# Performance work log

Measured on AMD Instinct MI355X. Metric: run time of the kernel, lower is better.

## Reference

```python
import jax, jax.numpy as jnp
import numpy as np

B, IN, H = 4096, 1024, 1024


def setup_inputs() -> dict:
    key = jax.random.key(0)
    ks = jax.random.split(key, 6)
    s_h = 1.0 / np.sqrt(H)
    s_x = 1.0 / np.sqrt(IN)
    return {
        "x": jax.random.normal(ks[0], (B, IN), jnp.float32),
        "h": jax.random.normal(ks[1], (B, H), jnp.float32),
        "c": jax.random.normal(ks[2], (B, H), jnp.float32),
        # hidden_lin: Linear(H, 4H) with bias
        "Wh": jax.random.uniform(ks[3], (4 * H, H), jnp.float32, -s_h, s_h),
        "bh": jax.random.uniform(ks[4], (4 * H,), jnp.float32, -s_h, s_h),
        # input_lin: Linear(IN, 4H), bias=False
        "Wx": jax.random.uniform(ks[5], (4 * H, IN), jnp.float32, -s_x, s_x),
    }


def reference(x, h, c, Wh, bh, Wx):
    # ifgo = h @ Wh^T + bh + x @ Wx^T   -> [B, 4H]
    ifgo = jnp.dot(h, Wh.T) + bh + jnp.dot(x, Wx.T)
    i, f, g, o = jnp.split(ifgo, 4, axis=1)
    i = jax.nn.sigmoid(i)
    f = jax.nn.sigmoid(f)
    g = jnp.tanh(g)
    o = jax.nn.sigmoid(o)
    c_next = f * c + i * g
    h_next = o * jnp.tanh(c_next)
    return (h_next, c_next)
```

## Files before the change

kernel.cpp:

```cpp
#include <hip/hip_runtime.h>
#include <cstdint>
#include <cstddef>


#define NB   4096
#define KH   1024
#define KK   2048
#define ARR_ELEMS 4194304
#define NKT  32

typedef __bf16 bf16x8 __attribute__((ext_vector_type(8)));
typedef float  f32x4  __attribute__((ext_vector_type(4)));

__device__ inline unsigned short f2bf(float f) {
    union { float f; unsigned int u; } v; v.f = f;
    unsigned int u = v.u;
    u += 0x7FFFu + ((u >> 16) & 1u);
    return (unsigned short)(u >> 16);
}

__device__ inline float fsig(float v)  { return __builtin_amdgcn_rcpf(1.f + __expf(-v)); }
__device__ inline float ftanh(float v) { return 1.f - 2.f * __builtin_amdgcn_rcpf(1.f + __expf(2.f * v)); }

__global__ void convert_kernel(const float* __restrict__ h, const float* __restrict__ x,
                               const float* __restrict__ Wh, const float* __restrict__ Wx,
                               unsigned short* __restrict__ A, unsigned short* __restrict__ W) {
    int idx = blockIdx.x * 256 + threadIdx.x;
    int arr = idx >> 19;
    int off = (idx & 0x7FFFF) << 3;
    const float* src = (arr == 0) ? h : (arr == 1) ? x : (arr == 2) ? Wh : Wx;
    float4 v0 = *(const float4*)(src + off);
    float4 v1 = *(const float4*)(src + off + 4);
    uint4 packed;
    packed.x = (unsigned int)f2bf(v0.x) | ((unsigned int)f2bf(v0.y) << 16);
    packed.y = (unsigned int)f2bf(v0.z) | ((unsigned int)f2bf(v0.w) << 16);
    packed.z = (unsigned int)f2bf(v1.x) | ((unsigned int)f2bf(v1.y) << 16);
    packed.w = (unsigned int)f2bf(v1.z) | ((unsigned int)f2bf(v1.w) << 16);

    int row = off >> 10;
    int col = off & 1023;
    unsigned short* dst;
    size_t dstOff;
    if (arr < 2) {
        dst = A;
        dstOff = (size_t)row * KK + (arr == 1 ? 1024 : 0) + col;
    } else {
        int g = row >> 10, j = row & 1023;
        int p = ((j >> 4) << 6) | (g << 4) | (j & 15);
        dst = W;
        dstOff = (size_t)p * KK + (arr == 3 ? 1024 : 0) + col;
    }
    *(uint4*)(dst + dstOff) = packed;
}

__global__ __launch_bounds__(512, 2) void gemm_kernel(const unsigned short* __restrict__ A,
                            const unsigned short* __restrict__ W,
                            const float* __restrict__ bh,
                            const float* __restrict__ c,
                            float* __restrict__ out) {
    __shared__ __align__(16) unsigned short As[2 * 16384];
    __shared__ __align__(16) unsigned short Bs[2 * 16384];

    const int tid  = threadIdx.x;
    const int wave = tid >> 6;
    const int lane = tid & 63;

    const int bid   = (int)blockIdx.x;
    const int swz   = (bid & 7) * 32 + (bid >> 3);
    const int tileM = swz >> 4;
    const int tileN = swz & 15;

    const int wr  = wave >> 2;
    const int wc  = wave & 3;
    const int fr  = lane & 15;
    const int fk2 = (lane >> 4) << 4;

    const unsigned short* pa[4];
    const unsigned short* pb[4];
    #pragma unroll
    for (int i = 0; i < 4; ++i) {
        const int P   = (i * 512 + tid) * 16;
        const int L   = P ^ (((P >> 7) & 7) << 4);
        const int row = L >> 7;
        const int kk  = (L & 127) >> 1;
        pa[i] = A + (size_t)(tileM * 256 + row) * KK + kk;
        pb[i] = W + (size_t)(tileN * 256 + row) * KK + kk;
    }

    const int swzm = (fr & 7) << 4;
    int offA[8], offB[4];
    #pragma unroll
    for (int i = 0; i < 8; ++i)
        offA[i] = (wr * 128 + i * 16 + fr) * 128 + (fk2 ^ swzm);
    #pragma unroll
    for (int j = 0; j < 4; ++j)
        offB[j] = (wc * 64 + j * 16 + fr) * 128 + (fk2 ^ swzm);

    f32x4 acc[8][4] = {};
    bf16x8 a03[4][2], a47[4][2], b01[2][2], b23[2][2];

#define STAGE(KT, BUF) do { \
    const size_t _ko = (size_t)(KT) * 64; \
    _Pragma("unroll") \
    for (int _i = 0; _i < 4; ++_i) { \
        __builtin_amdgcn_global_load_lds( \
            (const __attribute__((address_space(1))) void*)(pa[_i] + _ko), \
            (__attribute__((address_space(3))) void*)(As + (BUF) * 16384 + _i * 4096 + wave * 512), 16, 0, 0); \
        __builtin_amdgcn_global_load_lds( \
            (const __attribute__((address_space(1))) void*)(pb[_i] + _ko), \
            (__attribute__((address_space(3))) void*)(Bs + (BUF) * 16384 + _i * 4096 + wave * 512), 16, 0, 0); \
    } \
} while (0)

#define READ_A(dst, base, AsB) do { \
    _Pragma("unroll") \
    for (int _i = 0; _i < 4; ++_i) { \
        dst[_i][0] = *(const bf16x8*)((AsB) + offA[(base) + _i]); \
        dst[_i][1] = *(const bf16x8*)((AsB) + (offA[(base) + _i] ^ 64)); \
    } \
} while (0)

#define READ_B(dst, base, BsB) do { \
    _Pragma("unroll") \
    for (int _j = 0; _j < 2; ++_j) { \
        dst[_j][0] = *(const bf16x8*)((BsB) + offB[(base) + _j]); \
        dst[_j][1] = *(const bf16x8*)((BsB) + (offB[(base) + _j] ^ 64)); \
    } \
} while (0)

#define MFMAQ(af, bf, IB, JB) do { \
    __builtin_amdgcn_s_setprio(1); \
    _Pragma("unroll") \
    for (int _i = 0; _i < 4; ++_i) \
        _Pragma("unroll") \
        for (int _j = 0; _j < 2; ++_j) \
            _Pragma("unroll") \
            for (int _s = 0; _s < 2; ++_s) \
                acc[(IB) + _i][(JB) + _j] = __builtin_amdgcn_mfma_f32_16x16x32_bf16( \
                    af[_i][_s], bf[_j][_s], acc[(IB) + _i][(JB) + _j], 0, 0, 0); \
    __builtin_amdgcn_s_setprio(0); \
} while (0)

#define TILEBODY(T, BUF) do { \
    const char* AsB = (const char*)As + (BUF) * 32768; \
    const char* BsB = (const char*)Bs + (BUF) * 32768; \
    READ_B(b01, 0, BsB); \
    READ_A(a03, 0, AsB); \
    READ_A(a47, 4, AsB); \
    MFMAQ(a03, b01, 0, 0); \
    READ_B(b23, 2, BsB); \
    MFMAQ(a47, b01, 4, 0); \
    MFMAQ(a47, b23, 4, 2); \
    asm volatile("s_waitcnt lgkmcnt(0)" ::: "memory"); \
    asm volatile("s_barrier" ::: "memory"); \
    { \
        const int _kt = ((T) + 2 <= NKT - 1) ? ((T) + 2) : (NKT - 1); \
        STAGE(_kt, BUF);    \
    } \
    asm volatile("s_waitcnt vmcnt(8)" ::: "memory"); \
    asm volatile("s_barrier" ::: "memory"); \
    MFMAQ(a03, b23, 0, 2); \
} while (0)

    STAGE(0, 0);
    STAGE(1, 1);
    asm volatile("s_waitcnt vmcnt(8)" ::: "memory");
    asm volatile("s_barrier" ::: "memory");

    for (int tt = 0; tt < NKT; tt += 2) {
        TILEBODY(tt, 0);
        TILEBODY(tt + 1, 1);
    }
#undef TILEBODY
#undef MFMAQ
#undef READ_A
#undef READ_B
#undef STAGE

    const int j = ((tileN * 4 + wc) << 4) | fr;
    const float bi  = bh[j];
    const float bff = bh[j + 1024];
    const float bg  = bh[j + 2048];
    const float bo  = bh[j + 3072];

    const int row0 = tileM * 256 + wr * 128 + (lane >> 4) * 4;

    float cv[8][4];
    #pragma unroll
    for (int i = 0; i < 8; ++i)
        #pragma unroll
        for (int r = 0; r < 4; ++r)
            cv[i][r] = c[(size_t)(row0 + i * 16 + r) * KH + j];

    #pragma unroll
    for (int i = 0; i < 8; ++i) {
        #pragma unroll
        for (int r = 0; r < 4; ++r) {
            const size_t idx = (size_t)(row0 + i * 16 + r) * KH + j;
            float iv = fsig(acc[i][0][r] + bi);
            float fv = fsig(acc[i][1][r] + bff);
            float gv = ftanh(acc[i][2][r] + bg);
            float ov = fsig(acc[i][3][r] + bo);
            float cn = fv * cv[i][r] + iv * gv;
            float hn = ov * ftanh(cn);
            out[idx] = hn;
            out[(size_t)ARR_ELEMS + idx] = cn;
        }
    }
}

extern "C" void kernel_launch(void* const* d_in, const int* in_sizes, int n_in,
                              void* d_out, int out_size, void* d_ws, size_t ws_size,
                              hipStream_t stream) {
    const float* x  = (const float*)d_in[0];
    const float* h  = (const float*)d_in[1];
    const float* c  = (const float*)d_in[2];
    const float* Wh = (const float*)d_in[3];
    const float* bh = (const float*)d_in[4];
    const float* Wx = (const float*)d_in[5];
    float* out = (float*)d_out;

    unsigned short* ws   = (unsigned short*)d_ws;
    unsigned short* Acat = ws;
    unsigned short* Wcat = ws + 2 * (size_t)ARR_ELEMS;

    convert_kernel<<<8192, 256, 0, stream>>>(h, x, Wh, Wx, Acat, Wcat);
    gemm_kernel<<<256, 512, 0, stream>>>(Acat, Wcat, bh, c, out);
}
```

Baseline: 194.8 us.

## Load A operand directly from global into registers, keep only B in LDS

A-matrix fragments now go straight from global memory into MFMA registers, so A no longer passes through shared memory. Only the B tile is staged to LDS with async global-to-LDS loads. The per-tile pipeline is reordered to prefetch the next A fragments and next B reads after a single barrier, and it now waits on vmcnt(0). This removes half the LDS traffic and footprint. The cost is that each of the four column waves fetches the same A rows from global/L2, and every tile waits for all outstanding vector loads to finish, which can expose memory latency.

After: 300.8 us. 1.54x slower.

```diff
diff --git a/kernel.cpp b/kernel.cpp
--- a/kernel.cpp
+++ b/kernel.cpp
@@ -58,7 +58,6 @@
                             const float* __restrict__ bh,
                             const float* __restrict__ c,
                             float* __restrict__ out) {
-    __shared__ __align__(16) unsigned short As[2 * 16384];
     __shared__ __align__(16) unsigned short Bs[2 * 16384];
 
     const int tid  = threadIdx.x;
@@ -73,9 +72,15 @@
     const int wr  = wave >> 2;
     const int wc  = wave & 3;
     const int fr  = lane & 15;
-    const int fk2 = (lane >> 4) << 4;
-
-    const unsigned short* pa[4];
+    const int fkE = (lane >> 4) * 8;
+    const int fk2 = fkE * 2;
+
+    const int rowBase = tileM * 256 + wr * 128;
+    const unsigned short* pA[8];
+    #pragma unroll
+    for (int i = 0; i < 8; ++i)
+        pA[i] = A + (size_t)(rowBase + i * 16 + fr) * KK + fkE;
+
     const unsigned short* pb[4];
     #pragma unroll
     for (int i = 0; i < 4; ++i) {
@@ -83,15 +88,11 @@
         const int L   = P ^ (((P >> 7) & 7) << 4);
         const int row = L >> 7;
         const int kk  = (L & 127) >> 1;
-        pa[i] = A + (size_t)(tileM * 256 + row) * KK + kk;
         pb[i] = W + (size_t)(tileN * 256 + row) * KK + kk;
     }
 
     const int swzm = (fr & 7) << 4;
-    int offA[8], offB[4];
-    #pragma unroll
-    for (int i = 0; i < 8; ++i)
-        offA[i] = (wr * 128 + i * 16 + fr) * 128 + (fk2 ^ swzm);
+    int offB[4];
     #pragma unroll
     for (int j = 0; j < 4; ++j)
         offB[j] = (wc * 64 + j * 16 + fr) * 128 + (fk2 ^ swzm);
@@ -103,28 +104,25 @@
     const size_t _ko = (size_t)(KT) * 64; \
     _Pragma("unroll") \
     for (int _i = 0; _i < 4; ++_i) { \
-        __builtin_amdgcn_global_load_lds( \
-            (const __attribute__((address_space(1))) void*)(pa[_i] + _ko), \
-            (__attribute__((address_space(3))) void*)(As + (BUF) * 16384 + _i * 4096 + wave * 512), 16, 0, 0); \
         __builtin_amdgcn_global_load_lds( \
             (const __attribute__((address_space(1))) void*)(pb[_i] + _ko), \
             (__attribute__((address_space(3))) void*)(Bs + (BUF) * 16384 + _i * 4096 + wave * 512), 16, 0, 0); \
     } \
 } while (0)
 
-#define READ_A(dst, base, AsB) do { \
+#define LOAD_A(dst, ibase, T) do { \
     _Pragma("unroll") \
     for (int _i = 0; _i < 4; ++_i) { \
-        dst[_i][0] = *(const bf16x8*)((AsB) + offA[(base) + _i]); \
-        dst[_i][1] = *(const bf16x8*)((AsB) + (offA[(base) + _i] ^ 64)); \
-    } \
-} while (0)
-
-#define READ_B(dst, base, BsB) do { \
+        dst[_i][0] = *(const bf16x8*)(pA[(ibase) + _i] + (T) * 64); \
+        dst[_i][1] = *(const bf16x8*)(pA[(ibase) + _i] + (T) * 64 + 32); \
+    } \
+} while (0)
+
+#define READ_B(dst, jbase, BsB) do { \
     _Pragma("unroll") \
     for (int _j = 0; _j < 2; ++_j) { \
-        dst[_j][0] = *(const bf16x8*)((BsB) + offB[(base) + _j]); \
-        dst[_j][1] = *(const bf16x8*)((BsB) + (offB[(base) + _j] ^ 64)); \
+        dst[_j][0] = *(const bf16x8*)((BsB) + offB[(jbase) + _j]); \
+        dst[_j][1] = *(const bf16x8*)((BsB) + (offB[(jbase) + _j] ^ 64)); \
     } \
 } while (0)
 
@@ -142,30 +140,32 @@
 } while (0)
 
 #define TILEBODY(T, BUF) do { \
-    const char* AsB = (const char*)As + (BUF) * 32768; \
     const char* BsB = (const char*)Bs + (BUF) * 32768; \
-    READ_B(b01, 0, BsB); \
-    READ_A(a03, 0, AsB); \
-    READ_A(a47, 4, AsB); \
+    const char* BsN = (const char*)Bs + (((BUF) ^ 1)) * 32768; \
+    READ_B(b23, 2, BsB); \
+    LOAD_A(a47, 4, T); \
     MFMAQ(a03, b01, 0, 0); \
-    READ_B(b23, 2, BsB); \
+    MFMAQ(a03, b23, 0, 2); \
     MFMAQ(a47, b01, 4, 0); \
-    MFMAQ(a47, b23, 4, 2); \
     asm volatile("s_waitcnt lgkmcnt(0)" ::: "memory"); \
+    asm volatile("s_waitcnt vmcnt(0)" ::: "memory"); \
     asm volatile("s_barrier" ::: "memory"); \
     { \
-        const int _kt = ((T) + 2 <= NKT - 1) ? ((T) + 2) : (NKT - 1); \
-        STAGE(_kt, BUF);    \
-    } \
-    asm volatile("s_waitcnt vmcnt(8)" ::: "memory"); \
-    asm volatile("s_barrier" ::: "memory"); \
-    MFMAQ(a03, b23, 0, 2); \
+        const int _kt2 = ((T) + 2 <= NKT - 1) ? ((T) + 2) : (NKT - 1); \
+        const int _kt1 = ((T) + 1 <= NKT - 1) ? ((T) + 1) : (NKT - 1); \
+        STAGE(_kt2, BUF);           \
+        LOAD_A(a03, 0, _kt1); \
+        READ_B(b01, 0, BsN); \
+    } \
+    MFMAQ(a47, b23, 4, 2); \
 } while (0)
 
     STAGE(0, 0);
     STAGE(1, 1);
-    asm volatile("s_waitcnt vmcnt(8)" ::: "memory");
+    asm volatile("s_waitcnt vmcnt(4)" ::: "memory");
     asm volatile("s_barrier" ::: "memory");
+    LOAD_A(a03, 0, 0);
+    READ_B(b01, 0, (const char*)Bs);
 
     for (int tt = 0; tt < NKT; tt += 2) {
         TILEBODY(tt, 0);
@@ -173,8 +173,8 @@
     }
 #undef TILEBODY
 #undef MFMAQ
-#undef READ_A
 #undef READ_B
+#undef LOAD_A
 #undef STAGE
 
     const int j = ((tileN * 4 + wc) << 4) | fr;
```

## Shrink GEMM block tile to 128x128 with four waves and larger grid

Applied to the files above, without the earlier changes.

Reduces the per-block tile from 256x256 with 8 waves to 128x128 with 4 waves, launching 1024 blocks instead of 256. The interleaved fragment-read/MFMA schedule and priority hints are replaced by a simple load-all then compute body. This aims to improve occupancy and load balance across CUs, at the cost of lower data reuse per block, more global/L2 traffic, and less overlap of LDS reads with MFMA.

New measurement: 201.3 us. 3.4% more time.

```diff
diff --git a/kernel.cpp b/kernel.cpp
--- a/kernel.cpp
+++ b/kernel.cpp
@@ -53,51 +53,49 @@
     *(uint4*)(dst + dstOff) = packed;
 }
 
-__global__ __launch_bounds__(512, 2) void gemm_kernel(const unsigned short* __restrict__ A,
+__global__ __launch_bounds__(256, 2) void gemm_kernel(const unsigned short* __restrict__ A,
                             const unsigned short* __restrict__ W,
                             const float* __restrict__ bh,
                             const float* __restrict__ c,
                             float* __restrict__ out) {
-    __shared__ __align__(16) unsigned short As[2 * 16384];
-    __shared__ __align__(16) unsigned short Bs[2 * 16384];
+    __shared__ __align__(16) unsigned short As[2 * 8192];
+    __shared__ __align__(16) unsigned short Bs[2 * 8192];
 
     const int tid  = threadIdx.x;
     const int wave = tid >> 6;
     const int lane = tid & 63;
 
     const int bid   = (int)blockIdx.x;
-    const int swz   = (bid & 7) * 32 + (bid >> 3);
-    const int tileM = swz >> 4;
-    const int tileN = swz & 15;
-
-    const int wr  = wave >> 2;
-    const int wc  = wave & 3;
+    const int swz   = (bid & 7) * 128 + (bid >> 3);
+    const int tileM = swz >> 5;
+    const int tileN = swz & 31;
+
+    const int mBase = (wave >> 1) * 64;
+    const int nBase = (wave & 1) * 64;
     const int fr  = lane & 15;
-    const int fk2 = (lane >> 4) << 4;
+    const int fk2 = ((lane >> 4) << 4);
 
     const unsigned short* pa[4];
     const unsigned short* pb[4];
     #pragma unroll
     for (int i = 0; i < 4; ++i) {
-        const int P   = (i * 512 + tid) * 16;
+        const int P   = (i * 256 + tid) * 16;
         const int L   = P ^ (((P >> 7) & 7) << 4);
         const int row = L >> 7;
         const int kk  = (L & 127) >> 1;
-        pa[i] = A + (size_t)(tileM * 256 + row) * KK + kk;
-        pb[i] = W + (size_t)(tileN * 256 + row) * KK + kk;
+        pa[i] = A + (size_t)(tileM * 128 + row) * KK + kk;
+        pb[i] = W + (size_t)(tileN * 128 + row) * KK + kk;
     }
 
     const int swzm = (fr & 7) << 4;
-    int offA[8], offB[4];
-    #pragma unroll
-    for (int i = 0; i < 8; ++i)
-        offA[i] = (wr * 128 + i * 16 + fr) * 128 + (fk2 ^ swzm);
-    #pragma unroll
-    for (int j = 0; j < 4; ++j)
-        offB[j] = (wc * 64 + j * 16 + fr) * 128 + (fk2 ^ swzm);
-
-    f32x4 acc[8][4] = {};
-    bf16x8 a03[4][2], a47[4][2], b01[2][2], b23[2][2];
+    int offA[4], offB[4];
+    #pragma unroll
+    for (int i = 0; i < 4; ++i) {
+        offA[i] = (mBase + i * 16 + fr) * 128 + (fk2 ^ swzm);
+        offB[i] = (nBase + i * 16 + fr) * 128 + (fk2 ^ swzm);
+    }
+
+    f32x4 acc[4][4] = {};
 
 #define STAGE(KT, BUF) do { \
     const size_t _ko = (size_t)(KT) * 64; \
@@ -105,52 +103,32 @@
     for (int _i = 0; _i < 4; ++_i) { \
         __builtin_amdgcn_global_load_lds( \
             (const __attribute__((address_space(1))) void*)(pa[_i] + _ko), \
-            (__attribute__((address_space(3))) void*)(As + (BUF) * 16384 + _i * 4096 + wave * 512), 16, 0, 0); \
+            (__attribute__((address_space(3))) void*)(As + (BUF) * 8192 + _i * 2048 + wave * 512), 16, 0, 0); \
         __builtin_amdgcn_global_load_lds( \
             (const __attribute__((address_space(1))) void*)(pb[_i] + _ko), \
-            (__attribute__((address_space(3))) void*)(Bs + (BUF) * 16384 + _i * 4096 + wave * 512), 16, 0, 0); \
+            (__attribute__((address_space(3))) void*)(Bs + (BUF) * 8192 + _i * 2048 + wave * 512), 16, 0, 0); \
     } \
 } while (0)
 
-#define READ_A(dst, base, AsB) do { \
+#define TILEBODY(T, BUF) do { \
+    const char* AsB = (const char*)As + (BUF) * 16384; \
+    const char* BsB = (const char*)Bs + (BUF) * 16384; \
+    bf16x8 a[4][2], b[4][2]; \
     _Pragma("unroll") \
-    for (int _i = 0; _i < 4; ++_i) { \
-        dst[_i][0] = *(const bf16x8*)((AsB) + offA[(base) + _i]); \
-        dst[_i][1] = *(const bf16x8*)((AsB) + (offA[(base) + _i] ^ 64)); \
+    for (int i = 0; i < 4; ++i) { \
+        a[i][0] = *(const bf16x8*)(AsB + offA[i]); \
+        a[i][1] = *(const bf16x8*)(AsB + (offA[i] ^ 64)); \
+        b[i][0] = *(const bf16x8*)(BsB + offB[i]); \
+        b[i][1] = *(const bf16x8*)(BsB + (offB[i] ^ 64)); \
     } \
-} while (0)
-
-#define READ_B(dst, base, BsB) do { \
     _Pragma("unroll") \
-    for (int _j = 0; _j < 2; ++_j) { \
-        dst[_j][0] = *(const bf16x8*)((BsB) + offB[(base) + _j]); \
-        dst[_j][1] = *(const bf16x8*)((BsB) + (offB[(base) + _j] ^ 64)); \
-    } \
-} while (0)
-
-#define MFMAQ(af, bf, IB, JB) do { \
-    __builtin_amdgcn_s_setprio(1); \
-    _Pragma("unroll") \
-    for (int _i = 0; _i < 4; ++_i) \
+    for (int i = 0; i < 4; ++i) \
         _Pragma("unroll") \
-        for (int _j = 0; _j < 2; ++_j) \
+        for (int j = 0; j < 4; ++j) \
             _Pragma("unroll") \
-            for (int _s = 0; _s < 2; ++_s) \
-                acc[(IB) + _i][(JB) + _j] = __builtin_amdgcn_mfma_f32_16x16x32_bf16( \
-                    af[_i][_s], bf[_j][_s], acc[(IB) + _i][(JB) + _j], 0, 0, 0); \
-    __builtin_amdgcn_s_setprio(0); \
-} while (0)
-
-#define TILEBODY(T, BUF) do { \
-    const char* AsB = (const char*)As + (BUF) * 32768; \
-    const char* BsB = (const char*)Bs + (BUF) * 32768; \
-    READ_B(b01, 0, BsB); \
-    READ_A(a03, 0, AsB); \
-    READ_A(a47, 4, AsB); \
-    MFMAQ(a03, b01, 0, 0); \
-    READ_B(b23, 2, BsB); \
-    MFMAQ(a47, b01, 4, 0); \
-    MFMAQ(a47, b23, 4, 2); \
+            for (int s = 0; s < 2; ++s) \
+                acc[i][j] = __builtin_amdgcn_mfma_f32_16x16x32_bf16( \
+                    a[i][s], b[j][s], acc[i][j], 0, 0, 0); \
     asm volatile("s_waitcnt lgkmcnt(0)" ::: "memory"); \
     asm volatile("s_barrier" ::: "memory"); \
     { \
@@ -159,7 +137,6 @@
     } \
     asm volatile("s_waitcnt vmcnt(8)" ::: "memory"); \
     asm volatile("s_barrier" ::: "memory"); \
-    MFMAQ(a03, b23, 0, 2); \
 } while (0)
 
     STAGE(0, 0);
@@ -172,28 +149,25 @@
         TILEBODY(tt + 1, 1);
     }
 #undef TILEBODY
-#undef MFMAQ
-#undef READ_A
-#undef READ_B
 #undef STAGE
 
-    const int j = ((tileN * 4 + wc) << 4) | fr;
+    const int j = ((tileN * 2 + (wave & 1)) << 4) | fr;
     const float bi  = bh[j];
     const float bff = bh[j + 1024];
     const float bg  = bh[j + 2048];
     const float bo  = bh[j + 3072];
 
-    const int row0 = tileM * 256 + wr * 128 + (lane >> 4) * 4;
-
-    float cv[8][4];
-    #pragma unroll
-    for (int i = 0; i < 8; ++i)
+    const int row0 = tileM * 128 + mBase + (lane >> 4) * 4;
+
+    float cv[4][4];
+    #pragma unroll
+    for (int i = 0; i < 4; ++i)
         #pragma unroll
         for (int r = 0; r < 4; ++r)
             cv[i][r] = c[(size_t)(row0 + i * 16 + r) * KH + j];
 
     #pragma unroll
-    for (int i = 0; i < 8; ++i) {
+    for (int i = 0; i < 4; ++i) {
         #pragma unroll
         for (int r = 0; r < 4; ++r) {
             const size_t idx = (size_t)(row0 + i * 16 + r) * KH + j;
@@ -225,5 +199,6 @@
     unsigned short* Wcat = ws + 2 * (size_t)ARR_ELEMS;
 
     convert_kernel<<<8192, 256, 0, stream>>>(h, x, Wh, Wx, Acat, Wcat);
-    gemm_kernel<<<256, 512, 0, stream>>>(Acat, Wcat, bh, c, out);
-}
+    dim3 grid(1024);
+    gemm_kernel<<<grid, 256, 0, stream>>>(Acat, Wcat, bh, c, out);
+}
```

## Split A/B staging into phased ping-pong schedule with per-phase barriers

Applied to the files above, without the earlier changes.

Restructures the GEMM main loop into four phases. A-tile loads for the next k-step and B-tile loads for two steps ahead are interleaved between MFMA quadrants, with barriers and a raised wave priority around each MFMA block. The intent is to spread global-to-LDS traffic across the tile and overlap it better with matrix math, in a ping-pong style. The cost is more barriers per tile and a delicate buffer-reuse ordering; A and B now run at different prefetch distances.

Measured after the change: 188.8 us. 3.1% less time.

```diff
diff --git a/kernel.cpp b/kernel.cpp
--- a/kernel.cpp
+++ b/kernel.cpp
@@ -99,17 +99,22 @@
     f32x4 acc[8][4] = {};
     bf16x8 a03[4][2], a47[4][2], b01[2][2], b23[2][2];
 
-#define STAGE(KT, BUF) do { \
+#define STAGE_A(H, KT, BUF) do { \
     const size_t _ko = (size_t)(KT) * 64; \
     _Pragma("unroll") \
-    for (int _i = 0; _i < 4; ++_i) { \
+    for (int _i = 2*(H); _i < 2*(H)+2; ++_i) \
         __builtin_amdgcn_global_load_lds( \
             (const __attribute__((address_space(1))) void*)(pa[_i] + _ko), \
             (__attribute__((address_space(3))) void*)(As + (BUF) * 16384 + _i * 4096 + wave * 512), 16, 0, 0); \
+} while (0)
+
+#define STAGE_B(H, KT, BUF) do { \
+    const size_t _ko = (size_t)(KT) * 64; \
+    _Pragma("unroll") \
+    for (int _i = 2*(H); _i < 2*(H)+2; ++_i) \
         __builtin_amdgcn_global_load_lds( \
             (const __attribute__((address_space(1))) void*)(pb[_i] + _ko), \
             (__attribute__((address_space(3))) void*)(Bs + (BUF) * 16384 + _i * 4096 + wave * 512), 16, 0, 0); \
-    } \
 } while (0)
 
 #define READ_A(dst, base, AsB) do { \
@@ -129,7 +134,6 @@
 } while (0)
 
 #define MFMAQ(af, bf, IB, JB) do { \
-    __builtin_amdgcn_s_setprio(1); \
     _Pragma("unroll") \
     for (int _i = 0; _i < 4; ++_i) \
         _Pragma("unroll") \
@@ -138,44 +142,63 @@
             for (int _s = 0; _s < 2; ++_s) \
                 acc[(IB) + _i][(JB) + _j] = __builtin_amdgcn_mfma_f32_16x16x32_bf16( \
                     af[_i][_s], bf[_j][_s], acc[(IB) + _i][(JB) + _j], 0, 0, 0); \
+} while (0)
+
+#define PH_TAIL(MF) \
+    __builtin_amdgcn_s_barrier(); \
+    asm volatile("s_waitcnt lgkmcnt(0)" ::: "memory"); \
+    __builtin_amdgcn_sched_barrier(0); \
+    __builtin_amdgcn_s_setprio(1); \
+    MF; \
     __builtin_amdgcn_s_setprio(0); \
-} while (0)
+    __builtin_amdgcn_s_barrier();
 
 #define TILEBODY(T, BUF) do { \
     const char* AsB = (const char*)As + (BUF) * 32768; \
     const char* BsB = (const char*)Bs + (BUF) * 32768; \
+    const int _t1 = ((T) + 1 <= NKT - 1) ? ((T) + 1) : (NKT - 1); \
+    const int _t2 = ((T) + 2 <= NKT - 1) ? ((T) + 2) : (NKT - 1); \
+     \
+    READ_A(a03, 0, AsB); \
     READ_B(b01, 0, BsB); \
-    READ_A(a03, 0, AsB); \
+    STAGE_A(0, _t1, (BUF) ^ 1); \
+    asm volatile("s_waitcnt lgkmcnt(8)" ::: "memory"); \
+    PH_TAIL(MFMAQ(a03, b01, 0, 0)) \
+     \
+    READ_B(b23, 2, BsB); \
+    STAGE_A(1, _t1, (BUF) ^ 1); \
+    PH_TAIL(MFMAQ(a03, b23, 0, 2)) \
+     \
     READ_A(a47, 4, AsB); \
-    MFMAQ(a03, b01, 0, 0); \
-    READ_B(b23, 2, BsB); \
+    PH_TAIL(MFMAQ(a47, b23, 4, 2)) \
+     \
+    STAGE_B(0, _t2, BUF); \
+    STAGE_B(1, _t2, BUF); \
+    __builtin_amdgcn_s_barrier(); \
+    __builtin_amdgcn_s_setprio(1); \
     MFMAQ(a47, b01, 4, 0); \
-    MFMAQ(a47, b23, 4, 2); \
-    asm volatile("s_waitcnt lgkmcnt(0)" ::: "memory"); \
-    asm volatile("s_barrier" ::: "memory"); \
-    { \
-        const int _kt = ((T) + 2 <= NKT - 1) ? ((T) + 2) : (NKT - 1); \
-        STAGE(_kt, BUF);    \
-    } \
-    asm volatile("s_waitcnt vmcnt(8)" ::: "memory"); \
-    asm volatile("s_barrier" ::: "memory"); \
-    MFMAQ(a03, b23, 0, 2); \
-} while (0)
-
-    STAGE(0, 0);
-    STAGE(1, 1);
-    asm volatile("s_waitcnt vmcnt(8)" ::: "memory");
-    asm volatile("s_barrier" ::: "memory");
+    __builtin_amdgcn_s_setprio(0); \
+    asm volatile("s_waitcnt vmcnt(4)" ::: "memory"); \
+    __builtin_amdgcn_s_barrier(); \
+} while (0)
+
+    STAGE_A(0, 0, 0); STAGE_A(1, 0, 0);
+    STAGE_B(0, 0, 0); STAGE_B(1, 0, 0);
+    STAGE_B(0, 1, 1); STAGE_B(1, 1, 1);
+    asm volatile("s_waitcnt vmcnt(4)" ::: "memory");
+    __builtin_amdgcn_s_barrier();
 
     for (int tt = 0; tt < NKT; tt += 2) {
         TILEBODY(tt, 0);
         TILEBODY(tt + 1, 1);
     }
 #undef TILEBODY
+#undef PH_TAIL
 #undef MFMAQ
 #undef READ_A
 #undef READ_B
-#undef STAGE
+#undef STAGE_A
+#undef STAGE_B
 
     const int j = ((tileN * 4 + wc) << 4) | fr;
     const float bi  = bh[j];
```
